# Performance work log

Hardware: AMD Instinct MI355X
Metric: run time of the kernel (lower is better)

Reference implementation:

```python
import jax, jax.numpy as jnp
import numpy as np

DIM = 256
P = 0.1            # trainable-drop-rate
TEMP = 0.2         # trainable-temp
K = round(DIM * P) # number of peeling iterations (26)


def setup_inputs() -> dict:
    key = jax.random.key(0)
    k1, k2, k3 = jax.random.split(key, 3)
    N = 300000
    feature = jax.random.normal(k1, (N, DIM), dtype=jnp.float32)
    # Linear(dim, dim) params; scaled like torch default init (~1/sqrt(dim))
    W = jax.random.normal(k2, (DIM, DIM), dtype=jnp.float32) / jnp.sqrt(DIM)
    b = jax.random.normal(k3, (DIM,), dtype=jnp.float32) / jnp.sqrt(DIM)
    return {"feature": feature, "W": W, "b": b}


def reference(feature, W, b):
    # mask = Linear(feature)
    mask = feature @ W.T + b  # [N, dim]

    def step(y, _):
        w = 1.0 - y                              # remaining (un-dropped) weight
        logits = (mask + jnp.log(w + 1e-12)) / TEMP
        y1 = jax.nn.softmax(logits, axis=1)      # stable: subtracts row max
        return y + y1 * w, None

    y, _ = jax.lax.scan(step, jnp.zeros_like(mask), None, length=K)
    soft_mask = (1.0 - y) / (1.0 - P)
    return feature * soft_mask
```

## Files before the change

### kernel.cpp

```cpp
#include <hip/hip_runtime.h>
#include <hip/hip_bf16.h>
#include <math.h>

typedef _Float16 f16x8 __attribute__((ext_vector_type(8)));
typedef _Float16 f16x4 __attribute__((ext_vector_type(4)));
typedef float    f32x4 __attribute__((ext_vector_type(4)));
typedef float    f32x2 __attribute__((ext_vector_type(2)));

#define DIMD    256
#define MT      64
#define BT      256
#define KSTEPS  26
#define EXP_C   7.2134752044448170f
#define INV_1MP 1.1111111111111112f

static __device__ __forceinline__ f32x2 pk_fma(f32x2 a, f32x2 b, f32x2 c) {
    f32x2 d;
    asm("v_pk_fma_f32 %0, %1, %2, %3" : "=v"(d) : "v"(a), "v"(b), "v"(c));
    return d;
}
static __device__ __forceinline__ f32x2 pk_mul(f32x2 a, f32x2 b) {
    f32x2 d;
    asm("v_pk_mul_f32 %0, %1, %2" : "=v"(d) : "v"(a), "v"(b));
    return d;
}
static __device__ __forceinline__ f32x2 pk_add(f32x2 a, f32x2 b) {
    f32x2 d;
    asm("v_pk_add_f32 %0, %1, %2" : "=v"(d) : "v"(a), "v"(b));
    return d;
}

template<int CTRL>
static __device__ __forceinline__ float dpp_ror(float s) {
    return __builtin_bit_cast(float, __builtin_amdgcn_update_dpp(
        0, __builtin_bit_cast(int, s), CTRL, 0xf, 0xf, false));
}
static __device__ __forceinline__ float row16_sum(float s) {
    s += dpp_ror<0x128>(s);
    s += dpp_ror<0x124>(s);
    s += dpp_ror<0x122>(s);
    s += dpp_ror<0x121>(s);
    return s;
}
static __device__ __forceinline__ float row16_max(float m) {
    m = fmaxf(m, dpp_ror<0x128>(m));
    m = fmaxf(m, dpp_ror<0x124>(m));
    m = fmaxf(m, dpp_ror<0x122>(m));
    m = fmaxf(m, dpp_ror<0x121>(m));
    return m;
}

__global__ __launch_bounds__(256)
void w_conv_kernel(const float* __restrict__ W, f16x8* __restrict__ ws) {
    int gid  = blockIdx.x * 256 + threadIdx.x;
    int tile = gid >> 6;
    int lane = gid & 63;
    int kt = tile >> 4, ct = tile & 15;
    int col = ct * 16 + (lane & 15);
    int k0  = kt * 32 + (lane >> 4) * 8;
    const float* wr = W + col * 256 + k0;
    float4 f01 = *(const float4*)wr;
    float4 f23 = *(const float4*)(wr + 4);
    float wv[8] = {f01.x, f01.y, f01.z, f01.w, f23.x, f23.y, f23.z, f23.w};
    f16x8 hi;
    #pragma unroll
    for (int j = 0; j < 8; ++j) hi[j] = (_Float16)wv[j];
    ws[tile * 64 + lane] = hi;
}

__global__ __launch_bounds__(BT, 4)
void sad_mfma_kernel(const float* __restrict__ feat,
                     const float* __restrict__ bias,
                     const f16x8* __restrict__ ws,
                     float* __restrict__ out,
                     int N)
{
    __shared__ __align__(16) unsigned char smem[MT * 512];

    const int tid  = threadIdx.x;
    const int lane = tid & 63;
    const int wv   = tid >> 6;
    const long long n0 = (long long)blockIdx.x * MT;

    const float4* fvec = (const float4*)feat;
    #pragma unroll
    for (int i = 0; i < 16; ++i) {
        int flat4 = i * BT + tid;
        int row = flat4 >> 6;
        int c4  = flat4 & 63;
        long long grow = n0 + row;
        if (grow >= N) grow = N - 1;
        float4 f = fvec[grow * 64 + c4];
        f16x4 h4;
        h4[0] = (_Float16)f.x; h4[1] = (_Float16)f.y;
        h4[2] = (_Float16)f.z; h4[3] = (_Float16)f.w;
        int off = row * 512 + ((c4 * 8) ^ ((row & 7) << 4));
        *(f16x4*)(smem + off) = h4;
    }
    __syncthreads();

    f32x4 acc[16];
    #pragma unroll
    for (int ct = 0; ct < 16; ++ct) {
        float b = bias[ct * 16 + (lane & 15)];
        acc[ct] = f32x4{b, b, b, b};
    }

    const int arow  = wv * 16 + (lane & 15);
    const int swzA  = (arow & 7) << 4;
    const int abase = arow * 512;
    const int kgrp  = (lane >> 4) * 16;

    #pragma unroll
    for (int kt = 0; kt < 8; ++kt) {
        int kbyte = kt * 64 + kgrp;
        f16x8 a8 = *(const f16x8*)(smem + abase + (kbyte ^ swzA));
        #pragma unroll
        for (int ct = 0; ct < 16; ++ct) {
            f16x8 bh = ws[(kt * 16 + ct) * 64 + lane];
            acc[ct] = __builtin_amdgcn_mfma_f32_16x16x32_f16(a8, bh, acc[ct], 0, 0, 0);
        }
    }

    float M[4];
    #pragma unroll
    for (int p = 0; p < 4; ++p) {
        float m = acc[0][p];
        #pragma unroll
        for (int ct = 1; ct < 16; ++ct) m = fmaxf(m, acc[ct][p]);
        M[p] = row16_max(m);
    }

    const f32x2 one2 = f32x2{1.0f, 1.0f};

    #pragma unroll 1
    for (int p = 0; p < 4; ++p) {
        f32x2 E[8], z[8];
        #pragma unroll
        for (int cc = 0; cc < 8; ++cc) {
            float d0 = acc[2 * cc][p]     - M[p];
            float d1 = acc[2 * cc + 1][p] - M[p];
            E[cc] = f32x2{__builtin_amdgcn_exp2f(d0 * EXP_C),
                          __builtin_amdgcn_exp2f(d1 * EXP_C)};
            z[cc] = f32x2{1.0f, 1.0f};
        }

        #pragma unroll 1
        for (int it = 0; it < KSTEPS; ++it) {
            f32x2 t[8];
            #pragma unroll
            for (int cc = 0; cc < 8; ++cc) {
                f32x2 z2 = pk_mul(z[cc], z[cc]);
                f32x2 z4 = pk_mul(z2, z2);
                f32x2 z5 = pk_mul(z4, z[cc]);
                t[cc] = pk_mul(E[cc], z5);
            }
            f32x2 s2 = pk_add(pk_add(pk_add(t[0], t[1]), pk_add(t[2], t[3])),
                              pk_add(pk_add(t[4], t[5]), pk_add(t[6], t[7])));
            float s = row16_sum(s2.x + s2.y);
            s = fmaxf(s, 1e-30f);
            float rinv = __builtin_amdgcn_rcpf(s);
            f32x2 nr = f32x2{-rinv, -rinv};
            #pragma unroll
            for (int cc = 0; cc < 8; ++cc) {
                f32x2 u = pk_mul(t[cc], z[cc]);
                z[cc] = pk_fma(u, nr, z[cc]);
            }
        }

        int row = wv * 16 + (lane >> 4) * 4 + p;
        long long grow = n0 + row;
        if (grow < N) {
            int swz = (row & 7) << 4;
            float* orow = out + grow * 256;
            #pragma unroll
            for (int cc = 0; cc < 8; ++cc) {
                #pragma unroll
                for (int h = 0; h < 2; ++h) {
                    int col = (2 * cc + h) * 16 + (lane & 15);
                    float zz = h ? z[cc].y : z[cc].x;
                    int off = row * 512 + ((col * 2) ^ swz);
                    float fval = (float)(*(const _Float16*)(smem + off));
                    orow[col] = fval * (zz * INV_1MP);
                }
            }
        }
    }
}

extern "C" void kernel_launch(void* const* d_in, const int* in_sizes, int n_in,
                              void* d_out, int out_size, void* d_ws, size_t ws_size,
                              hipStream_t stream) {
    const float* feat = (const float*)d_in[0];
    const float* W    = (const float*)d_in[1];
    const float* bias = (const float*)d_in[2];
    float* out = (float*)d_out;
    int N = in_sizes[0] / DIMD;

    w_conv_kernel<<<32, 256, 0, stream>>>(W, (f16x8*)d_ws);

    int grid = (int)((N + MT - 1) / MT);
    sad_mfma_kernel<<<grid, BT, 0, stream>>>(feat, bias, (const f16x8*)d_ws, out, N);
}
```

Baseline: 343.5 us.

## Track softmax numerators instead of remaining weights and process two rows per loop

The peeling iteration is reformulated to carry q = E*z^5 directly, so each step computes the row sum straight from q and updates q via r=1-q/s, q*=r^5. The remaining weight z is recovered at the end with a log/exp2 from q and the original logits. Two rows are interleaved in the inner loop for ILP, packed-f32 inline asm is dropped, and the occupancy hint rises to 5 blocks per CU. The reformulation risks precision loss when q underflows, which the 1e-38 clamp only partly handles.

```diff
diff --git a/kernel.cpp b/kernel.cpp
--- a/kernel.cpp
+++ b/kernel.cpp
@@ -5,30 +5,14 @@
 typedef _Float16 f16x8 __attribute__((ext_vector_type(8)));
 typedef _Float16 f16x4 __attribute__((ext_vector_type(4)));
 typedef float    f32x4 __attribute__((ext_vector_type(4)));
-typedef float    f32x2 __attribute__((ext_vector_type(2)));
 
 #define DIMD    256
 #define MT      64
 #define BT      256
 #define KSTEPS  26
 #define EXP_C   7.2134752044448170f
+#define LOG2E   1.4426950408889634f
 #define INV_1MP 1.1111111111111112f
-
-static __device__ __forceinline__ f32x2 pk_fma(f32x2 a, f32x2 b, f32x2 c) {
-    f32x2 d;
-    asm("v_pk_fma_f32 %0, %1, %2, %3" : "=v"(d) : "v"(a), "v"(b), "v"(c));
-    return d;
-}
-static __device__ __forceinline__ f32x2 pk_mul(f32x2 a, f32x2 b) {
-    f32x2 d;
-    asm("v_pk_mul_f32 %0, %1, %2" : "=v"(d) : "v"(a), "v"(b));
-    return d;
-}
-static __device__ __forceinline__ f32x2 pk_add(f32x2 a, f32x2 b) {
-    f32x2 d;
-    asm("v_pk_add_f32 %0, %1, %2" : "=v"(d) : "v"(a), "v"(b));
-    return d;
-}
 
 template<int CTRL>
 static __device__ __forceinline__ float dpp_ror(float s) {
@@ -68,7 +52,7 @@
     ws[tile * 64 + lane] = hi;
 }
 
-__global__ __launch_bounds__(BT, 4)
+__global__ __launch_bounds__(BT, 5)
 void sad_mfma_kernel(const float* __restrict__ feat,
                      const float* __restrict__ bias,
                      const f16x8* __restrict__ ws,
@@ -131,54 +115,62 @@
         M[p] = row16_max(m);
     }
 
-    const f32x2 one2 = f32x2{1.0f, 1.0f};
+    #pragma unroll
+    for (int pp = 0; pp < 2; ++pp) {
+        const int p0 = 2 * pp, p1 = p0 + 1;
 
-    #pragma unroll 1
-    for (int p = 0; p < 4; ++p) {
-        f32x2 E[8], z[8];
+        float qa[16], qb[16];
         #pragma unroll
-        for (int cc = 0; cc < 8; ++cc) {
-            float d0 = acc[2 * cc][p]     - M[p];
-            float d1 = acc[2 * cc + 1][p] - M[p];
-            E[cc] = f32x2{__builtin_amdgcn_exp2f(d0 * EXP_C),
-                          __builtin_amdgcn_exp2f(d1 * EXP_C)};
-            z[cc] = f32x2{1.0f, 1.0f};
+        for (int j = 0; j < 16; ++j) {
+            qa[j] = __builtin_amdgcn_exp2f((acc[j][p0] - M[p0]) * EXP_C);
+            qb[j] = __builtin_amdgcn_exp2f((acc[j][p1] - M[p1]) * EXP_C);
         }
 
         #pragma unroll 1
         for (int it = 0; it < KSTEPS; ++it) {
-            f32x2 t[8];
+            float sa0 = ((qa[0] + qa[1]) + (qa[2] + qa[3]))
+                      + ((qa[4] + qa[5]) + (qa[6] + qa[7]));
+            float sa1 = ((qa[8] + qa[9]) + (qa[10] + qa[11]))
+                      + ((qa[12] + qa[13]) + (qa[14] + qa[15]));
+            float sb0 = ((qb[0] + qb[1]) + (qb[2] + qb[3]))
+                      + ((qb[4] + qb[5]) + (qb[6] + qb[7]));
+            float sb1 = ((qb[8] + qb[9]) + (qb[10] + qb[11]))
+                      + ((qb[12] + qb[13]) + (qb[14] + qb[15]));
+            float sa = row16_sum(sa0 + sa1);
+            float sb = row16_sum(sb0 + sb1);
+            sa = fmaxf(sa, 1e-30f);
+            sb = fmaxf(sb, 1e-30f);
+            float na = -__builtin_amdgcn_rcpf(sa);
+            float nb = -__builtin_amdgcn_rcpf(sb);
             #pragma unroll
-            for (int cc = 0; cc < 8; ++cc) {
-                f32x2 z2 = pk_mul(z[cc], z[cc]);
-                f32x2 z4 = pk_mul(z2, z2);
-                f32x2 z5 = pk_mul(z4, z[cc]);
-                t[cc] = pk_mul(E[cc], z5);
-            }
-            f32x2 s2 = pk_add(pk_add(pk_add(t[0], t[1]), pk_add(t[2], t[3])),
-                              pk_add(pk_add(t[4], t[5]), pk_add(t[6], t[7])));
-            float s = row16_sum(s2.x + s2.y);
-            s = fmaxf(s, 1e-30f);
-            float rinv = __builtin_amdgcn_rcpf(s);
-            f32x2 nr = f32x2{-rinv, -rinv};
-            #pragma unroll
-            for (int cc = 0; cc < 8; ++cc) {
-                f32x2 u = pk_mul(t[cc], z[cc]);
-                z[cc] = pk_fma(u, nr, z[cc]);
+            for (int j = 0; j < 16; ++j) {
+                float ra  = fmaf(qa[j], na, 1.0f);
+                float rb  = fmaf(qb[j], nb, 1.0f);
+                float ra2 = ra * ra;
+                float rb2 = rb * rb;
+                float ra4 = ra2 * ra2;
+                float rb4 = rb2 * rb2;
+                qa[j] *= ra4 * ra;
+                qb[j] *= rb4 * rb;
             }
         }
 
-        int row = wv * 16 + (lane >> 4) * 4 + p;
-        long long grow = n0 + row;
-        if (grow < N) {
-            int swz = (row & 7) << 4;
-            float* orow = out + grow * 256;
-            #pragma unroll
-            for (int cc = 0; cc < 8; ++cc) {
+        #pragma unroll
+        for (int half = 0; half < 2; ++half) {
+            int p = half ? p1 : p0;
+            const float* q = half ? qb : qa;
+            int row = wv * 16 + (lane >> 4) * 4 + p;
+            long long grow = n0 + row;
+            if (grow < N) {
+                int swz = (row & 7) << 4;
+                float* orow = out + grow * 256;
                 #pragma unroll
-                for (int h = 0; h < 2; ++h) {
-                    int col = (2 * cc + h) * 16 + (lane & 15);
-                    float zz = h ? z[cc].y : z[cc].x;
+                for (int j = 0; j < 16; ++j) {
+                    int col = j * 16 + (lane & 15);
+                    float le5 = (acc[j][p] - M[p]) * LOG2E;
+                    float qv  = fmaxf(q[j], 1e-38f);
+                    float zz  = __builtin_amdgcn_exp2f(
+                        fmaf(__builtin_amdgcn_logf(qv), 0.2f, -le5));
                     int off = row * 512 + ((col * 2) ^ swz);
                     float fval = (float)(*(const _Float16*)(smem + off));
                     orow[col] = fval * (zz * INV_1MP);
```

Measured after the change: 399.2 us. 1.16x slower.
